# Kernel tuning notes

Measured on AMD Instinct MI355X. Metric: run time of the kernel, lower is better.

## Reference

```python
import jax, jax.numpy as jnp
import numpy as np

EPS = 1e-5

def layer_norm(x, g, b):
    mu = jnp.mean(x, axis=-1, keepdims=True)
    var = jnp.mean(jnp.square(x - mu), axis=-1, keepdims=True)
    return (x - mu) * jax.lax.rsqrt(var + EPS) * g + b

def setup_inputs() -> dict:
    key = jax.random.key(0)
    ks = jax.random.split(key, 10)
    B, V, S, D, H, FF = 4, 1024, 2048, 512, 8, 2048
    s = 0.02
    return {
        "tgt": jax.random.normal(ks[0], (B, V, D), jnp.float32),
        "memory": jax.random.normal(ks[1], (B, S, D), jnp.float32),
        "memory_key_padding_mask": jax.random.bernoulli(ks[2], 0.3, (B, S)),  # True = padding
        "Wq": jax.random.normal(ks[3], (D, D), jnp.float32) * s,
        "Wkv": jax.random.normal(ks[4], (2 * D, D), jnp.float32) * s,
        "Wo": jax.random.normal(ks[5], (D, D), jnp.float32) * s,
        "W1": jax.random.normal(ks[6], (FF, D), jnp.float32) * s,
        "b1": jnp.zeros((FF,), jnp.float32),
        "W2": jax.random.normal(ks[7], (D, FF), jnp.float32) * s,
        "b2": jnp.zeros((D,), jnp.float32),
        "g1": jnp.ones((D,), jnp.float32),
        "be1": jnp.zeros((D,), jnp.float32),
        "g2": jnp.ones((D,), jnp.float32),
        "be2": jnp.zeros((D,), jnp.float32),
    }

def reference(tgt, memory, memory_key_padding_mask, Wq, Wkv, Wo, W1, b1, W2, b2, g1, be1, g2, be2):
    B, V, D = tgt.shape
    S = memory.shape[1]
    H = 8
    hd = D // H
    # projections (no bias on q/kv/out per bias=False)
    q = (tgt @ Wq.T).reshape(B, V, H, hd)
    kv = (memory @ Wkv.T).reshape(B, S, 2, H, hd)
    k, v = kv[:, :, 0], kv[:, :, 1]
    # cross attention over valid (non-padded) context tokens only.
    # Equivalent math to flash-attn-varlen packing: padded keys get zero weight.
    scores = jnp.einsum("bqhd,bkhd->bhqk", q, k) / jnp.sqrt(jnp.asarray(hd, q.dtype))
    neg = jnp.finfo(scores.dtype).min
    scores = jnp.where(memory_key_padding_mask[:, None, None, :], neg, scores)
    attn = jax.nn.softmax(scores, axis=-1)
    attn_out = jnp.einsum("bhqk,bkhd->bqhd", attn, v).reshape(B, V, D)
    attn_out = attn_out @ Wo.T
    # post-norm scheme, dropout=0
    x = layer_norm(tgt + attn_out, g1, be1)
    ff = jax.nn.relu(x @ W1.T + b1) @ W2.T + b2
    return layer_norm(x + ff, g2, be2)
```

## Files before the change

### kernel.cpp

```cpp
#include <hip/hip_runtime.h>
#include <hip/hip_bf16.h>

typedef unsigned short u16;
typedef __attribute__((ext_vector_type(8))) short short8;
typedef __attribute__((ext_vector_type(4))) float floatx4;

#define AS1 __attribute__((address_space(1)))
#define AS3 __attribute__((address_space(3)))

__device__ __forceinline__ u16 f2bf(float f) {
  unsigned u = __float_as_uint(f);
  u = u + 0x7FFFu + ((u >> 16) & 1u);
  return (u16)(u >> 16);
}
__device__ __forceinline__ unsigned pack_bf2(float a, float b) {
  return (unsigned)f2bf(a) | ((unsigned)f2bf(b) << 16);
}

__global__ __launch_bounds__(256) void cast_bf16_kernel(const float* __restrict__ in,
                                                        u16* __restrict__ out, int n4) {
  int i = blockIdx.x * 256 + threadIdx.x;
  int stride = gridDim.x * 256;
  for (; i < n4; i += stride) {
    float4 v = reinterpret_cast<const float4*>(in)[i];
    ushort4 o;
    o.x = f2bf(v.x); o.y = f2bf(v.y); o.z = f2bf(v.z); o.w = f2bf(v.w);
    reinterpret_cast<ushort4*>(out)[i] = o;
  }
}

__global__ __launch_bounds__(256) void mask_bits_kernel(const void* __restrict__ mraw,
                                                        unsigned* __restrict__ mout, int n) {
  __shared__ int mode;
  const int t = threadIdx.x;
  const int* mi = (const int*)mraw;
  if (t == 0) mode = 0;
  __syncthreads();
  int local = 0;
  for (int i = t; i < 2048; i += 256) {
    unsigned v = (unsigned)mi[i];
    if (v == 0x3F800000u) { local = 2; break; }
    if (v > 1u) local = 1;
  }
  atomicMax(&mode, local);
  __syncthreads();
  const int m = mode;
  const unsigned char* mb = (const unsigned char*)mraw;
  const float* mf = (const float*)mraw;
  for (int wk = t; wk < n / 32; wk += 256) {
    unsigned bits = 0;
    for (int i = 0; i < 32; ++i) {
      int s = wk * 32 + i;
      int v;
      if (m == 1)      v = (int)mb[s];
      else if (m == 2) v = (mf[s] != 0.0f) ? 1 : 0;
      else             v = mi[s];
      bits |= (v ? 1u : 0u) << i;
    }
    mout[wk] = bits;
  }
}

template<int EPI>
__global__ __launch_bounds__(256) void gemm_bt(
    const u16* __restrict__ A, const u16* __restrict__ B, void* __restrict__ Cv,
    const float* __restrict__ bias,
    int M, int N, int K, int lda, int ldb, int ldc,
    long aBatch, long bBatch, long cBatch)
{
  __shared__ u16 As[2][128 * 32];
  __shared__ u16 Bs[2][128 * 32];
  const int t = threadIdx.x;
  const int l = t & 63;
  const int w = t >> 6;
  const int wr = w >> 1, wc = w & 1;
  const int m0 = blockIdx.y * 128, n0 = blockIdx.x * 128;
  const long z = blockIdx.z;
  const u16* Ab = A + z * aBatch;
  const u16* Bb = B + z * bBatch;

  floatx4 acc[4][4];
#pragma unroll
  for (int m = 0; m < 4; ++m)
#pragma unroll
    for (int n = 0; n < 4; ++n)
      acc[m][n] = (floatx4){0.f, 0.f, 0.f, 0.f};

  const int row_st = t >> 2;
  const int kcol = (t & 3) * 8;

  auto stage = [&](int buf, int kt) {
#pragma unroll
    for (int c = 0; c < 2; ++c) {
      int rA = m0 + c * 64 + row_st; if (rA >= M) rA = M - 1;
      int rB = n0 + c * 64 + row_st; if (rB >= N) rB = N - 1;
      int li = (c * 256 + t) * 8;
      __builtin_amdgcn_global_load_lds(
          (const AS1 void*)(Ab + (long)rA * lda + kt + kcol),
          (AS3 void*)(As[buf] + li), 16, 0, 0);
      __builtin_amdgcn_global_load_lds(
          (const AS1 void*)(Bb + (long)rB * ldb + kt + kcol),
          (AS3 void*)(Bs[buf] + li), 16, 0, 0);
    }
  };

  stage(0, 0);
  __syncthreads();
  int cur = 0;
  for (int kt = 0; kt < K; kt += 32) {
    if (kt + 32 < K) stage(cur ^ 1, kt + 32);

    short8 af[4], bf[4];
#pragma unroll
    for (int m = 0; m < 4; ++m)
      af[m] = *reinterpret_cast<const short8*>(&As[cur][(wr * 64 + m * 16 + (l & 15)) * 32 + (l >> 4) * 8]);
#pragma unroll
    for (int n = 0; n < 4; ++n)
      bf[n] = *reinterpret_cast<const short8*>(&Bs[cur][(wc * 64 + n * 16 + (l & 15)) * 32 + (l >> 4) * 8]);

    __builtin_amdgcn_s_setprio(1);
#pragma unroll
    for (int m = 0; m < 4; ++m)
#pragma unroll
      for (int n = 0; n < 4; ++n)
        acc[m][n] = __builtin_amdgcn_mfma_f32_16x16x32_bf16(af[m], bf[n], acc[m][n], 0, 0, 0);
    __builtin_amdgcn_s_setprio(0);

    __syncthreads();
    cur ^= 1;
  }

  const int cr = (l >> 4) * 4;
  const int cc = l & 15;
#pragma unroll
  for (int m = 0; m < 4; ++m) {
#pragma unroll
    for (int j = 0; j < 4; ++j) {
      int row = m0 + wr * 64 + m * 16 + cr + j;
      if (row < M) {
#pragma unroll
        for (int n = 0; n < 4; ++n) {
          int col = n0 + wc * 64 + n * 16 + cc;
          if (col < N) {
            float v = acc[m][n][j];
            long idx = z * cBatch + (long)row * ldc + col;
            if constexpr (EPI == 0) {
              ((u16*)Cv)[idx] = f2bf(v);
            } else if constexpr (EPI == 1) {
              ((float*)Cv)[idx] = v;
            } else if constexpr (EPI == 2) {
              v += bias[col]; v = fmaxf(v, 0.f);
              ((u16*)Cv)[idx] = f2bf(v);
            } else {
              v += bias[col];
              ((float*)Cv)[idx] = v;
            }
          }
        }
      }
    }
  }
}

__global__ __launch_bounds__(512, 4) void flash_attn_kernel(
    const u16* __restrict__ Qg, const u16* __restrict__ KVg,
    const u16* __restrict__ Vtg, const unsigned* __restrict__ mbits,
    u16* __restrict__ Og)
{
  __shared__ __align__(16) u16 KVbuf[2][2][64 * 64];
  __shared__ __align__(16) u16 Ps[8][32 * 32];
  __shared__ float mlred[2][2][128];
  __shared__ unsigned mw[64];

  const int t = threadIdx.x;
  const int l = t & 63;
  const int w = t >> 6;
  const int wr = w >> 1;
  const int wc = w & 1;
  const int lo = l & 15, hi = l >> 4;

  const int id = blockIdx.y * 8 + blockIdx.x;
  const int vid = (id & 7) * 32 + (id >> 3);
  const int qt = vid & 7, bh = vid >> 3;
  const int b = bh >> 3, h = bh & 7;

  const long qbase = ((long)b * 1024 + qt * 128) * 512 + h * 64;
  const long kbase = ((long)b * 2048) * 1024 + h * 64;
  const long vbase = ((long)bh * 64) * 2048;

  if (t < 64) mw[t] = mbits[b * 64 + t];

  auto stage_kv = [&](int buf, int soff) {
    const int s = t >> 3, c = t & 7;
    __builtin_amdgcn_global_load_lds(
        (const AS1 void*)(KVg + kbase + (long)(soff + s) * 1024 + ((c ^ (s & 7)) * 8)),
        (AS3 void*)(&KVbuf[buf][0][t * 8]), 16, 0, 0);
    __builtin_amdgcn_global_load_lds(
        (const AS1 void*)(Vtg + vbase + (long)s * 2048 + soff + ((c ^ (s & 7)) * 8)),
        (AS3 void*)(&KVbuf[buf][1][t * 8]), 16, 0, 0);
  };

  stage_kv(0, 0);

  short8 af[2][2];
#pragma unroll
  for (int qm = 0; qm < 2; ++qm)
#pragma unroll
    for (int ks = 0; ks < 2; ++ks)
      af[qm][ks] = *reinterpret_cast<const short8*>(
          Qg + qbase + (long)(wr * 32 + qm * 16 + lo) * 512 + ks * 32 + hi * 8);

  __syncthreads();

  floatx4 accO[4][2];
#pragma unroll
  for (int dn = 0; dn < 4; ++dn)
#pragma unroll
    for (int qm = 0; qm < 2; ++qm)
      accO[dn][qm] = (floatx4){0.f, 0.f, 0.f, 0.f};
  float m_run[2] = {-1.0e30f, -1.0e30f};
  float l_run[2] = {0.f, 0.f};

  int cur = 0;
  for (int it = 0; it < 32; ++it) {
    const int s0 = it * 64;
    if (it + 1 < 32) stage_kv(cur ^ 1, s0 + 64);

    short8 bfr[2][2];
#pragma unroll
    for (int sn = 0; sn < 2; ++sn)
#pragma unroll
      for (int ks = 0; ks < 2; ++ks) {
        const int srow = wc * 32 + sn * 16 + lo;
        bfr[sn][ks] = *reinterpret_cast<const short8*>(
            &KVbuf[cur][0][srow * 64 + (((ks * 4 + hi) ^ (lo & 7)) * 8)]);
      }
    floatx4 sacc[2][2];
#pragma unroll
    for (int sn = 0; sn < 2; ++sn)
#pragma unroll
      for (int qm = 0; qm < 2; ++qm)
        sacc[sn][qm] = (floatx4){0.f, 0.f, 0.f, 0.f};
    __builtin_amdgcn_s_setprio(1);
#pragma unroll
    for (int sn = 0; sn < 2; ++sn)
#pragma unroll
      for (int qm = 0; qm < 2; ++qm)
#pragma unroll
        for (int ks = 0; ks < 2; ++ks)
          sacc[sn][qm] = __builtin_amdgcn_mfma_f32_16x16x32_bf16(bfr[sn][ks], af[qm][ks], sacc[sn][qm], 0, 0, 0);
    __builtin_amdgcn_s_setprio(0);

    const unsigned mword = mw[it * 2 + wc];
#pragma unroll
    for (int sn = 0; sn < 2; ++sn) {
      const unsigned nib = (mword >> (sn * 16)) >> (hi * 4);
#pragma unroll
      for (int j = 0; j < 4; ++j) {
        const bool mk = (nib >> j) & 1u;
#pragma unroll
        for (int qm = 0; qm < 2; ++qm)
          sacc[sn][qm][j] = mk ? -3.0e38f : sacc[sn][qm][j] * 0.125f;
      }
    }

    float al[2];
#pragma unroll
    for (int qm = 0; qm < 2; ++qm) {
      float mx = fmaxf(fmaxf(fmaxf(sacc[0][qm][0], sacc[0][qm][1]), fmaxf(sacc[0][qm][2], sacc[0][qm][3])),
                       fmaxf(fmaxf(sacc[1][qm][0], sacc[1][qm][1]), fmaxf(sacc[1][qm][2], sacc[1][qm][3])));
      mx = fmaxf(mx, __shfl_xor(mx, 16));
      mx = fmaxf(mx, __shfl_xor(mx, 32));
      const float mn = fmaxf(m_run[qm], mx);
      al[qm] = __expf(m_run[qm] - mn);
      m_run[qm] = mn;
      l_run[qm] *= al[qm];
    }
#pragma unroll
    for (int dn = 0; dn < 4; ++dn)
#pragma unroll
      for (int qm = 0; qm < 2; ++qm)
#pragma unroll
        for (int j = 0; j < 4; ++j)
          accO[dn][qm][j] *= al[qm];

#pragma unroll
    for (int qm = 0; qm < 2; ++qm) {
      float s = 0.f;
      unsigned pw[2][2];
#pragma unroll
      for (int sn = 0; sn < 2; ++sn) {
        const float e0 = __expf(sacc[sn][qm][0] - m_run[qm]);
        const float e1 = __expf(sacc[sn][qm][1] - m_run[qm]);
        const float e2 = __expf(sacc[sn][qm][2] - m_run[qm]);
        const float e3 = __expf(sacc[sn][qm][3] - m_run[qm]);
        s += (e0 + e1) + (e2 + e3);
        pw[sn][0] = pack_bf2(e0, e1);
        pw[sn][1] = pack_bf2(e2, e3);
      }
      s += __shfl_xor(s, 16);
      s += __shfl_xor(s, 32);
      l_run[qm] += s;
      const int ql = qm * 16 + lo;
#pragma unroll
      for (int sn = 0; sn < 2; ++sn) {
        uint2 wv; wv.x = pw[sn][0]; wv.y = pw[sn][1];
        *reinterpret_cast<uint2*>(&Ps[w][ql * 32 + (((sn * 4 + hi) ^ (lo & 7)) * 4)]) = wv;
      }
    }

    short8 va[4];
#pragma unroll
    for (int dn = 0; dn < 4; ++dn) {
      const int d = dn * 16 + lo;
      va[dn] = *reinterpret_cast<const short8*>(
          &KVbuf[cur][1][d * 64 + (((wc * 4 + hi) ^ (d & 7)) * 8)]);
    }
    short8 pb[2];
#pragma unroll
    for (int qm = 0; qm < 2; ++qm) {
      const int ql = qm * 16 + lo;
      uint2 a = *reinterpret_cast<const uint2*>(&Ps[w][ql * 32 + (((2 * hi) ^ (lo & 7)) * 4)]);
      uint2 bq = *reinterpret_cast<const uint2*>(&Ps[w][ql * 32 + (((2 * hi + 1) ^ (lo & 7)) * 4)]);
      uint4 comb; comb.x = a.x; comb.y = a.y; comb.z = bq.x; comb.w = bq.y;
      __builtin_memcpy(&pb[qm], &comb, 16);
    }
    __builtin_amdgcn_s_setprio(1);
#pragma unroll
    for (int dn = 0; dn < 4; ++dn)
#pragma unroll
      for (int qm = 0; qm < 2; ++qm)
        accO[dn][qm] = __builtin_amdgcn_mfma_f32_16x16x32_bf16(va[dn], pb[qm], accO[dn][qm], 0, 0, 0);
    __builtin_amdgcn_s_setprio(0);

    __syncthreads();
    cur ^= 1;
  }

  if (hi == 0) {
#pragma unroll
    for (int qm = 0; qm < 2; ++qm) {
      const int q = wr * 32 + qm * 16 + lo;
      mlred[wc][0][q] = m_run[qm];
      mlred[wc][1][q] = l_run[qm];
    }
  }
  __syncthreads();
  float scal[2];
#pragma unroll
  for (int qm = 0; qm < 2; ++qm) {
    const int q = wr * 32 + qm * 16 + lo;
    const float ms = fmaxf(mlred[0][0][q], mlred[1][0][q]);
    scal[qm] = __expf(m_run[qm] - ms);
  }
  float* Of = (float*)KVbuf;
  if (wc == 0) {
#pragma unroll
    for (int dn = 0; dn < 4; ++dn)
#pragma unroll
      for (int qm = 0; qm < 2; ++qm) {
        const int q = wr * 32 + qm * 16 + lo;
        float4 v;
        v.x = accO[dn][qm][0] * scal[qm]; v.y = accO[dn][qm][1] * scal[qm];
        v.z = accO[dn][qm][2] * scal[qm]; v.w = accO[dn][qm][3] * scal[qm];
        *reinterpret_cast<float4*>(&Of[q * 64 + (((dn * 4 + hi) ^ (q & 15)) * 4)]) = v;
      }
  }
  __syncthreads();
  if (wc == 1) {
#pragma unroll
    for (int dn = 0; dn < 4; ++dn)
#pragma unroll
      for (int qm = 0; qm < 2; ++qm) {
        const int q = wr * 32 + qm * 16 + lo;
        float4* pp = reinterpret_cast<float4*>(&Of[q * 64 + (((dn * 4 + hi) ^ (q & 15)) * 4)]);
        float4 v = *pp;
        v.x += accO[dn][qm][0] * scal[qm]; v.y += accO[dn][qm][1] * scal[qm];
        v.z += accO[dn][qm][2] * scal[qm]; v.w += accO[dn][qm][3] * scal[qm];
        *pp = v;
      }
  }
  __syncthreads();
  {
    const int q = t >> 2;
    const float m0 = mlred[0][0][q], m1 = mlred[1][0][q];
    const float ms = fmaxf(m0, m1);
    const float ls = mlred[0][1][q] * __expf(m0 - ms) + mlred[1][1][q] * __expf(m1 - ms);
    const float inv = 1.0f / ls;
    u16 ov[16];
#pragma unroll
    for (int c4 = 0; c4 < 4; ++c4) {
      const int c = (t & 3) * 4 + c4;
      float4 v = *reinterpret_cast<const float4*>(&Of[q * 64 + ((c ^ (q & 15)) * 4)]);
      ov[c4 * 4 + 0] = f2bf(v.x * inv); ov[c4 * 4 + 1] = f2bf(v.y * inv);
      ov[c4 * 4 + 2] = f2bf(v.z * inv); ov[c4 * 4 + 3] = f2bf(v.w * inv);
    }
    u16* dst = Og + qbase + (long)q * 512 + (t & 3) * 16;
    uint4 w0, w1;
    __builtin_memcpy(&w0, &ov[0], 16);
    __builtin_memcpy(&w1, &ov[8], 16);
    *reinterpret_cast<uint4*>(dst) = w0;
    *reinterpret_cast<uint4*>(dst + 8) = w1;
  }
}

template<int P, bool WRITE_BF>
__global__ __launch_bounds__(64) void lnp_kernel(const float* __restrict__ r1,
    const float* __restrict__ parts, long pstride,
    const float* __restrict__ bias,
    const float* __restrict__ g, const float* __restrict__ be,
    float* __restrict__ xf, u16* __restrict__ xb) {
  const long base = (long)blockIdx.x * 512;
  const int t = threadIdx.x;
  float v[8]; float s = 0.f;
#pragma unroll
  for (int j = 0; j < 8; ++j) {
    int i = t + j * 64;
    float acc = r1[base + i] + (bias ? bias[i] : 0.f);
#pragma unroll
    for (int q = 0; q < P; ++q) acc += parts[q * pstride + base + i];
    v[j] = acc; s += acc;
  }
#pragma unroll
  for (int o = 32; o; o >>= 1) s += __shfl_xor(s, o);
  const float mu = s * (1.0f / 512.0f);
  float q2 = 0.f;
#pragma unroll
  for (int j = 0; j < 8; ++j) { float d = v[j] - mu; q2 += d * d; }
#pragma unroll
  for (int o = 32; o; o >>= 1) q2 += __shfl_xor(q2, o);
  const float rs = rsqrtf(q2 * (1.0f / 512.0f) + 1e-5f);
#pragma unroll
  for (int j = 0; j < 8; ++j) {
    int i = t + j * 64;
    float o = (v[j] - mu) * rs * g[i] + be[i];
    xf[base + i] = o;
    if (WRITE_BF) xb[base + i] = f2bf(o);
  }
}

__global__ __launch_bounds__(256) void transpose_v_kernel(const u16* __restrict__ KV,
                                                          u16* __restrict__ Vt) {
  __shared__ u16 tile[128 * 65];
  const int z = blockIdx.y;
  const int b = z >> 3, h = z & 7;
  const int s0 = blockIdx.x * 128;
  const int t = threadIdx.x;
#pragma unroll
  for (int k = 0; k < 32; ++k) {
    int i = k * 256 + t;
    int s = i >> 6, d = i & 63;
    tile[s * 65 + d] = KV[(long)(b * 2048 + s0 + s) * 1024 + 512 + h * 64 + d];
  }
  __syncthreads();
#pragma unroll
  for (int k = 0; k < 32; ++k) {
    int i = k * 256 + t;
    int d = i >> 7, sl = i & 127;
    Vt[((long)z * 64 + d) * 2048 + s0 + sl] = tile[sl * 65 + d];
  }
}

extern "C" void kernel_launch(void* const* d_in, const int* in_sizes, int n_in,
                              void* d_out, int out_size, void* d_ws, size_t ws_size,
                              hipStream_t stream) {
  const float* tgt    = (const float*)d_in[0];
  const float* memory = (const float*)d_in[1];
  const void*  maskraw= (const void*)d_in[2];
  const float* Wq  = (const float*)d_in[3];
  const float* Wkv = (const float*)d_in[4];
  const float* Wo  = (const float*)d_in[5];
  const float* W1  = (const float*)d_in[6];
  const float* b1  = (const float*)d_in[7];
  const float* W2  = (const float*)d_in[8];
  const float* b2  = (const float*)d_in[9];
  const float* g1  = (const float*)d_in[10];
  const float* be1 = (const float*)d_in[11];
  const float* g2  = (const float*)d_in[12];
  const float* be2 = (const float*)d_in[13];

  constexpr int B = 4, V = 1024, S = 2048, D = 512, H = 8, FF = 2048, hd = 64;
  const long BVD = (long)B * V * D;

  char* p = (char*)d_ws;
  auto alloc = [&](size_t bytes) -> void* {
    void* r = (void*)p; p += (bytes + 255) & ~(size_t)255; return r;
  };
  u16*  tgt_b = (u16*)alloc((size_t)B * V * D * 2);
  u16*  mem_b = (u16*)alloc((size_t)B * S * D * 2);
  u16*  wq_b  = (u16*)alloc((size_t)D * D * 2);
  u16*  wkv_b = (u16*)alloc((size_t)2 * D * D * 2);
  u16*  wo_b  = (u16*)alloc((size_t)D * D * 2);
  u16*  w1_b  = (u16*)alloc((size_t)FF * D * 2);
  u16*  w2_b  = (u16*)alloc((size_t)D * FF * 2);
  u16*  Qb    = (u16*)alloc((size_t)B * V * D * 2);
  u16*  KVb   = (u16*)alloc((size_t)B * S * 2 * D * 2);
  u16*  Vt    = (u16*)alloc((size_t)B * H * hd * S * 2);
  u16*  attn_b= (u16*)alloc((size_t)B * V * D * 2);
  float* projP = (float*)alloc((size_t)4 * BVD * 4);
  float* xf   = (float*)alloc((size_t)BVD * 4);
  u16*  xb    = (u16*)alloc((size_t)BVD * 2);
  u16*  hb    = (u16*)alloc((size_t)B * V * FF * 2);
  float* ffbP = (float*)alloc((size_t)4 * BVD * 4);
  unsigned* mbitsW = (unsigned*)alloc((size_t)(B * S / 32) * 4);

  auto cast = [&](const float* src, u16* dst, long n) {
    int n4 = (int)(n / 4);
    int grid = (n4 + 255) / 256; if (grid > 2048) grid = 2048; if (grid < 1) grid = 1;
    cast_bf16_kernel<<<dim3(grid), dim3(256), 0, stream>>>(src, dst, n4);
  };
  cast(tgt, tgt_b, (long)B * V * D);
  cast(memory, mem_b, (long)B * S * D);
  cast(Wq, wq_b, (long)D * D);
  cast(Wkv, wkv_b, (long)2 * D * D);
  cast(Wo, wo_b, (long)D * D);
  cast(W1, w1_b, (long)FF * D);
  cast(W2, w2_b, (long)D * FF);

  mask_bits_kernel<<<dim3(1), 256, 0, stream>>>(maskraw, mbitsW, B * S);

  gemm_bt<0><<<dim3(D / 128, (B * V) / 128, 1), 256, 0, stream>>>(
      tgt_b, wq_b, Qb, nullptr, B * V, D, D, D, D, D, 0, 0, 0);
  gemm_bt<0><<<dim3((2 * D) / 128, (B * S) / 128, 1), 256, 0, stream>>>(
      mem_b, wkv_b, KVb, nullptr, B * S, 2 * D, D, D, D, 2 * D, 0, 0, 0);
  transpose_v_kernel<<<dim3(S / 128, B * H), 256, 0, stream>>>(KVb, Vt);

  flash_attn_kernel<<<dim3(8, B * H), 512, 0, stream>>>(
      Qb, KVb, Vt, mbitsW, attn_b);

  gemm_bt<1><<<dim3(D / 128, (B * V) / 128, 4), 256, 0, stream>>>(
      attn_b, wo_b, projP, nullptr, B * V, D, D / 4, D, D, D,
      (long)(D / 4), (long)(D / 4), BVD);
  lnp_kernel<4, true><<<dim3(B * V), 64, 0, stream>>>(
      tgt, projP, BVD, nullptr, g1, be1, xf, xb);
  gemm_bt<2><<<dim3(FF / 128, (B * V) / 128, 1), 256, 0, stream>>>(
      xb, w1_b, hb, b1, B * V, FF, D, D, D, FF, 0, 0, 0);
  gemm_bt<1><<<dim3(D / 128, (B * V) / 128, 4), 256, 0, stream>>>(
      hb, w2_b, ffbP, nullptr, B * V, D, FF / 4, FF, FF, D,
      (long)(FF / 4), (long)(FF / 4), BVD);
  lnp_kernel<4, false><<<dim3(B * V), 64, 0, stream>>>(
      xf, ffbP, BVD, b2, g2, be2, (float*)d_out, nullptr);
}
```

Before: 302.8 us.

## Halve attention query tile, fold softmax scale into Q GEMM, merge cast launches

```diff
diff --git a/kernel.cpp b/kernel.cpp
--- a/kernel.cpp
+++ b/kernel.cpp
@@ -1,5 +1,4 @@
 #include <hip/hip_runtime.h>
-#include <hip/hip_bf16.h>
 
 typedef unsigned short u16;
 typedef __attribute__((ext_vector_type(8))) short short8;
@@ -17,15 +16,31 @@
   return (unsigned)f2bf(a) | ((unsigned)f2bf(b) << 16);
 }
 
-__global__ __launch_bounds__(256) void cast_bf16_kernel(const float* __restrict__ in,
-                                                        u16* __restrict__ out, int n4) {
+__global__ __launch_bounds__(256) void cast_all_kernel(
+    const float* __restrict__ s0, u16* __restrict__ d0,
+    const float* __restrict__ s1, u16* __restrict__ d1,
+    const float* __restrict__ s2, u16* __restrict__ d2,
+    const float* __restrict__ s3, u16* __restrict__ d3,
+    const float* __restrict__ s4, u16* __restrict__ d4,
+    const float* __restrict__ s5, u16* __restrict__ d5,
+    const float* __restrict__ s6, u16* __restrict__ d6)
+{
+  const int total = 2359296;
   int i = blockIdx.x * 256 + threadIdx.x;
-  int stride = gridDim.x * 256;
-  for (; i < n4; i += stride) {
-    float4 v = reinterpret_cast<const float4*>(in)[i];
+  const int stride = gridDim.x * 256;
+  for (; i < total; i += stride) {
+    const float* s; u16* d; int loc;
+    if (i < 524288)        { s = s0; d = d0; loc = i; }
+    else if (i < 1572864)  { s = s1; d = d1; loc = i - 524288; }
+    else if (i < 1638400)  { s = s2; d = d2; loc = i - 1572864; }
+    else if (i < 1769472)  { s = s3; d = d3; loc = i - 1638400; }
+    else if (i < 1835008)  { s = s4; d = d4; loc = i - 1769472; }
+    else if (i < 2097152)  { s = s5; d = d5; loc = i - 1835008; }
+    else                   { s = s6; d = d6; loc = i - 2097152; }
+    float4 v = reinterpret_cast<const float4*>(s)[loc];
     ushort4 o;
     o.x = f2bf(v.x); o.y = f2bf(v.y); o.z = f2bf(v.z); o.w = f2bf(v.w);
-    reinterpret_cast<ushort4*>(out)[i] = o;
+    reinterpret_cast<ushort4*>(d)[loc] = o;
   }
 }
 
@@ -45,17 +60,28 @@
   atomicMax(&mode, local);
   __syncthreads();
   const int m = mode;
-  const unsigned char* mb = (const unsigned char*)mraw;
-  const float* mf = (const float*)mraw;
-  for (int wk = t; wk < n / 32; wk += 256) {
+  const uint4* m4 = (const uint4*)mraw;
+  const int nw = n / 32;
+  for (int wk = t; wk < nw; wk += 256) {
     unsigned bits = 0;
-    for (int i = 0; i < 32; ++i) {
-      int s = wk * 32 + i;
-      int v;
-      if (m == 1)      v = (int)mb[s];
-      else if (m == 2) v = (mf[s] != 0.0f) ? 1 : 0;
-      else             v = mi[s];
-      bits |= (v ? 1u : 0u) << i;
+    if (m == 1) {
+      uint4 a = m4[wk * 2], b = m4[wk * 2 + 1];
+      unsigned ww[8] = {a.x, a.y, a.z, a.w, b.x, b.y, b.z, b.w};
+#pragma unroll
+      for (int k = 0; k < 8; ++k)
+#pragma unroll
+        for (int j = 0; j < 4; ++j)
+          bits |= (((ww[k] >> (j * 8)) & 0xFFu) ? 1u : 0u) << (k * 4 + j);
+    } else {
+#pragma unroll
+      for (int k = 0; k < 8; ++k) {
+        uint4 a = m4[wk * 8 + k];
+        unsigned t0 = (m == 2) ? ((a.x << 1) ? 1u : 0u) : (a.x ? 1u : 0u);
+        unsigned t1 = (m == 2) ? ((a.y << 1) ? 1u : 0u) : (a.y ? 1u : 0u);
+        unsigned t2 = (m == 2) ? ((a.z << 1) ? 1u : 0u) : (a.z ? 1u : 0u);
+        unsigned t3 = (m == 2) ? ((a.w << 1) ? 1u : 0u) : (a.w ? 1u : 0u);
+        bits |= (t0 | (t1 << 1) | (t2 << 2) | (t3 << 3)) << (k * 4);
+      }
     }
     mout[wk] = bits;
   }
@@ -92,9 +118,9 @@
   auto stage = [&](int buf, int kt) {
 #pragma unroll
     for (int c = 0; c < 2; ++c) {
-      int rA = m0 + c * 64 + row_st; if (rA >= M) rA = M - 1;
-      int rB = n0 + c * 64 + row_st; if (rB >= N) rB = N - 1;
-      int li = (c * 256 + t) * 8;
+      const int rA = m0 + c * 64 + row_st;
+      const int rB = n0 + c * 64 + row_st;
+      const int li = (c * 256 + t) * 8;
       __builtin_amdgcn_global_load_lds(
           (const AS1 void*)(Ab + (long)rA * lda + kt + kcol),
           (AS3 void*)(As[buf] + li), 16, 0, 0);
@@ -136,26 +162,24 @@
   for (int m = 0; m < 4; ++m) {
 #pragma unroll
     for (int j = 0; j < 4; ++j) {
-      int row = m0 + wr * 64 + m * 16 + cr + j;
-      if (row < M) {
-#pragma unroll
-        for (int n = 0; n < 4; ++n) {
-          int col = n0 + wc * 64 + n * 16 + cc;
-          if (col < N) {
-            float v = acc[m][n][j];
-            long idx = z * cBatch + (long)row * ldc + col;
-            if constexpr (EPI == 0) {
-              ((u16*)Cv)[idx] = f2bf(v);
-            } else if constexpr (EPI == 1) {
-              ((float*)Cv)[idx] = v;
-            } else if constexpr (EPI == 2) {
-              v += bias[col]; v = fmaxf(v, 0.f);
-              ((u16*)Cv)[idx] = f2bf(v);
-            } else {
-              v += bias[col];
-              ((float*)Cv)[idx] = v;
-            }
-          }
+      const int row = m0 + wr * 64 + m * 16 + cr + j;
+#pragma unroll
+      for (int n = 0; n < 4; ++n) {
+        const int col = n0 + wc * 64 + n * 16 + cc;
+        float v = acc[m][n][j];
+        long idx = z * cBatch + (long)row * ldc + col;
+        if constexpr (EPI == 0) {
+          ((u16*)Cv)[idx] = f2bf(v);
+        } else if constexpr (EPI == 1) {
+          ((float*)Cv)[idx] = v;
+        } else if constexpr (EPI == 2) {
+          v += bias[col]; v = fmaxf(v, 0.f);
+          ((u16*)Cv)[idx] = f2bf(v);
+        } else if constexpr (EPI == 3) {
+          v += bias[col];
+          ((float*)Cv)[idx] = v;
+        } else {
+          ((u16*)Cv)[idx] = f2bf(v * 0.125f);
         }
       }
     }
@@ -168,8 +192,8 @@
     u16* __restrict__ Og)
 {
   __shared__ __align__(16) u16 KVbuf[2][2][64 * 64];
-  __shared__ __align__(16) u16 Ps[8][32 * 32];
-  __shared__ float mlred[2][2][128];
+  __shared__ __align__(16) u16 Ps[8][16 * 32];
+  __shared__ float mlred[2][2][64];
   __shared__ unsigned mw[64];
 
   const int t = threadIdx.x;
@@ -179,12 +203,12 @@
   const int wc = w & 1;
   const int lo = l & 15, hi = l >> 4;
 
-  const int id = blockIdx.y * 8 + blockIdx.x;
-  const int vid = (id & 7) * 32 + (id >> 3);
-  const int qt = vid & 7, bh = vid >> 3;
+  const int id = blockIdx.y * 16 + blockIdx.x;
+  const int vid = (id & 7) * 64 + (id >> 3);
+  const int qt = vid & 15, bh = vid >> 4;
   const int b = bh >> 3, h = bh & 7;
 
-  const long qbase = ((long)b * 1024 + qt * 128) * 512 + h * 64;
+  const long qbase = ((long)b * 1024 + qt * 64) * 512 + h * 64;
   const long kbase = ((long)b * 2048) * 1024 + h * 64;
   const long vbase = ((long)bh * 64) * 2048;
 
@@ -202,24 +226,19 @@
 
   stage_kv(0, 0);
 
-  short8 af[2][2];
-#pragma unroll
-  for (int qm = 0; qm < 2; ++qm)
-#pragma unroll
-    for (int ks = 0; ks < 2; ++ks)
-      af[qm][ks] = *reinterpret_cast<const short8*>(
-          Qg + qbase + (long)(wr * 32 + qm * 16 + lo) * 512 + ks * 32 + hi * 8);
-
-  __syncthreads();
-
-  floatx4 accO[4][2];
+  short8 af[2];
+#pragma unroll
+  for (int ks = 0; ks < 2; ++ks)
+    af[ks] = *reinterpret_cast<const short8*>(
+        Qg + qbase + (long)(wr * 16 + lo) * 512 + ks * 32 + hi * 8);
+
+  __syncthreads();
+
+  floatx4 accO[4];
 #pragma unroll
   for (int dn = 0; dn < 4; ++dn)
-#pragma unroll
-    for (int qm = 0; qm < 2; ++qm)
-      accO[dn][qm] = (floatx4){0.f, 0.f, 0.f, 0.f};
-  float m_run[2] = {-1.0e30f, -1.0e30f};
-  float l_run[2] = {0.f, 0.f};
+    accO[dn] = (floatx4){0.f, 0.f, 0.f, 0.f};
+  float m_run = -1.0e30f, l_run = 0.f;
 
   int cur = 0;
   for (int it = 0; it < 32; ++it) {
@@ -235,20 +254,16 @@
         bfr[sn][ks] = *reinterpret_cast<const short8*>(
             &KVbuf[cur][0][srow * 64 + (((ks * 4 + hi) ^ (lo & 7)) * 8)]);
       }
-    floatx4 sacc[2][2];
+    floatx4 sacc[2];
 #pragma unroll
     for (int sn = 0; sn < 2; ++sn)
-#pragma unroll
-      for (int qm = 0; qm < 2; ++qm)
-        sacc[sn][qm] = (floatx4){0.f, 0.f, 0.f, 0.f};
+      sacc[sn] = (floatx4){0.f, 0.f, 0.f, 0.f};
     __builtin_amdgcn_s_setprio(1);
 #pragma unroll
     for (int sn = 0; sn < 2; ++sn)
 #pragma unroll
-      for (int qm = 0; qm < 2; ++qm)
-#pragma unroll
-        for (int ks = 0; ks < 2; ++ks)
-          sacc[sn][qm] = __builtin_amdgcn_mfma_f32_16x16x32_bf16(bfr[sn][ks], af[qm][ks], sacc[sn][qm], 0, 0, 0);
+      for (int ks = 0; ks < 2; ++ks)
+        sacc[sn] = __builtin_amdgcn_mfma_f32_16x16x32_bf16(bfr[sn][ks], af[ks], sacc[sn], 0, 0, 0);
     __builtin_amdgcn_s_setprio(0);
 
     const unsigned mword = mw[it * 2 + wc];
@@ -256,56 +271,44 @@
     for (int sn = 0; sn < 2; ++sn) {
       const unsigned nib = (mword >> (sn * 16)) >> (hi * 4);
 #pragma unroll
-      for (int j = 0; j < 4; ++j) {
-        const bool mk = (nib >> j) & 1u;
-#pragma unroll
-        for (int qm = 0; qm < 2; ++qm)
-          sacc[sn][qm][j] = mk ? -3.0e38f : sacc[sn][qm][j] * 0.125f;
-      }
-    }
-
-    float al[2];
-#pragma unroll
-    for (int qm = 0; qm < 2; ++qm) {
-      float mx = fmaxf(fmaxf(fmaxf(sacc[0][qm][0], sacc[0][qm][1]), fmaxf(sacc[0][qm][2], sacc[0][qm][3])),
-                       fmaxf(fmaxf(sacc[1][qm][0], sacc[1][qm][1]), fmaxf(sacc[1][qm][2], sacc[1][qm][3])));
-      mx = fmaxf(mx, __shfl_xor(mx, 16));
-      mx = fmaxf(mx, __shfl_xor(mx, 32));
-      const float mn = fmaxf(m_run[qm], mx);
-      al[qm] = __expf(m_run[qm] - mn);
-      m_run[qm] = mn;
-      l_run[qm] *= al[qm];
-    }
+      for (int j = 0; j < 4; ++j)
+        if ((nib >> j) & 1u) sacc[sn][j] = -3.0e38f;
+    }
+
+    float mx = fmaxf(fmaxf(fmaxf(sacc[0][0], sacc[0][1]), fmaxf(sacc[0][2], sacc[0][3])),
+                     fmaxf(fmaxf(sacc[1][0], sacc[1][1]), fmaxf(sacc[1][2], sacc[1][3])));
+    mx = fmaxf(mx, __shfl_xor(mx, 16));
+    mx = fmaxf(mx, __shfl_xor(mx, 32));
+    const float mn = fmaxf(m_run, mx);
+    const float al = __expf(m_run - mn);
+    m_run = mn;
+    l_run *= al;
 #pragma unroll
     for (int dn = 0; dn < 4; ++dn)
 #pragma unroll
-      for (int qm = 0; qm < 2; ++qm)
-#pragma unroll
-        for (int j = 0; j < 4; ++j)
-          accO[dn][qm][j] *= al[qm];
-
-#pragma unroll
-    for (int qm = 0; qm < 2; ++qm) {
+      for (int j = 0; j < 4; ++j)
+        accO[dn][j] *= al;
+
+    {
       float s = 0.f;
       unsigned pw[2][2];
 #pragma unroll
       for (int sn = 0; sn < 2; ++sn) {
-        const float e0 = __expf(sacc[sn][qm][0] - m_run[qm]);
-        const float e1 = __expf(sacc[sn][qm][1] - m_run[qm]);
-        const float e2 = __expf(sacc[sn][qm][2] - m_run[qm]);
-        const float e3 = __expf(sacc[sn][qm][3] - m_run[qm]);
+        const float e0 = __expf(sacc[sn][0] - m_run);
+        const float e1 = __expf(sacc[sn][1] - m_run);
+        const float e2 = __expf(sacc[sn][2] - m_run);
+        const float e3 = __expf(sacc[sn][3] - m_run);
         s += (e0 + e1) + (e2 + e3);
         pw[sn][0] = pack_bf2(e0, e1);
         pw[sn][1] = pack_bf2(e2, e3);
       }
       s += __shfl_xor(s, 16);
       s += __shfl_xor(s, 32);
-      l_run[qm] += s;
-      const int ql = qm * 16 + lo;
+      l_run += s;
 #pragma unroll
       for (int sn = 0; sn < 2; ++sn) {
         uint2 wv; wv.x = pw[sn][0]; wv.y = pw[sn][1];
-        *reinterpret_cast<uint2*>(&Ps[w][ql * 32 + (((sn * 4 + hi) ^ (lo & 7)) * 4)]) = wv;
+        *reinterpret_cast<uint2*>(&Ps[w][lo * 32 + (((sn * 4 + hi) ^ (lo & 7)) * 4)]) = wv;
       }
     }
 
@@ -316,21 +319,17 @@
       va[dn] = *reinterpret_cast<const short8*>(
           &KVbuf[cur][1][d * 64 + (((wc * 4 + hi) ^ (d & 7)) * 8)]);
     }
-    short8 pb[2];
-#pragma unroll
-    for (int qm = 0; qm < 2; ++qm) {
-      const int ql = qm * 16 + lo;
-      uint2 a = *reinterpret_cast<const uint2*>(&Ps[w][ql * 32 + (((2 * hi) ^ (lo & 7)) * 4)]);
-      uint2 bq = *reinterpret_cast<const uint2*>(&Ps[w][ql * 32 + (((2 * hi + 1) ^ (lo & 7)) * 4)]);
+    short8 pb;
+    {
+      uint2 a = *reinterpret_cast<const uint2*>(&Ps[w][lo * 32 + (((2 * hi) ^ (lo & 7)) * 4)]);
+      uint2 bq = *reinterpret_cast<const uint2*>(&Ps[w][lo * 32 + (((2 * hi + 1) ^ (lo & 7)) * 4)]);
       uint4 comb; comb.x = a.x; comb.y = a.y; comb.z = bq.x; comb.w = bq.y;
-      __builtin_memcpy(&pb[qm], &comb, 16);
+      __builtin_memcpy(&pb, &comb, 16);
     }
     __builtin_amdgcn_s_setprio(1);
 #pragma unroll
     for (int dn = 0; dn < 4; ++dn)
-#pragma unroll
-      for (int qm = 0; qm < 2; ++qm)
-        accO[dn][qm] = __builtin_amdgcn_mfma_f32_16x16x32_bf16(va[dn], pb[qm], accO[dn][qm], 0, 0, 0);
+      accO[dn] = __builtin_amdgcn_mfma_f32_16x16x32_bf16(va[dn], pb, accO[dn], 0, 0, 0);
     __builtin_amdgcn_s_setprio(0);
 
     __syncthreads();
@@ -338,69 +337,58 @@
   }
 
   if (hi == 0) {
-#pragma unroll
-    for (int qm = 0; qm < 2; ++qm) {
-      const int q = wr * 32 + qm * 16 + lo;
-      mlred[wc][0][q] = m_run[qm];
-      mlred[wc][1][q] = l_run[qm];
-    }
-  }
-  __syncthreads();
-  float scal[2];
-#pragma unroll
-  for (int qm = 0; qm < 2; ++qm) {
-    const int q = wr * 32 + qm * 16 + lo;
+    const int q = wr * 16 + lo;
+    mlred[wc][0][q] = m_run;
+    mlred[wc][1][q] = l_run;
+  }
+  __syncthreads();
+  float scal;
+  {
+    const int q = wr * 16 + lo;
     const float ms = fmaxf(mlred[0][0][q], mlred[1][0][q]);
-    scal[qm] = __expf(m_run[qm] - ms);
+    scal = __expf(m_run - ms);
   }
   float* Of = (float*)KVbuf;
   if (wc == 0) {
 #pragma unroll
-    for (int dn = 0; dn < 4; ++dn)
-#pragma unroll
-      for (int qm = 0; qm < 2; ++qm) {
-        const int q = wr * 32 + qm * 16 + lo;
-        float4 v;
-        v.x = accO[dn][qm][0] * scal[qm]; v.y = accO[dn][qm][1] * scal[qm];
-        v.z = accO[dn][qm][2] * scal[qm]; v.w = accO[dn][qm][3] * scal[qm];
-        *reinterpret_cast<float4*>(&Of[q * 64 + (((dn * 4 + hi) ^ (q & 15)) * 4)]) = v;
-      }
+    for (int dn = 0; dn < 4; ++dn) {
+      const int q = wr * 16 + lo;
+      float4 v;
+      v.x = accO[dn][0] * scal; v.y = accO[dn][1] * scal;
+      v.z = accO[dn][2] * scal; v.w = accO[dn][3] * scal;
+      *reinterpret_cast<float4*>(&Of[q * 64 + (((dn * 4 + hi) ^ (q & 15)) * 4)]) = v;
+    }
   }
   __syncthreads();
   if (wc == 1) {
 #pragma unroll
-    for (int dn = 0; dn < 4; ++dn)
-#pragma unroll
-      for (int qm = 0; qm < 2; ++qm) {
-        const int q = wr * 32 + qm * 16 + lo;
-        float4* pp = reinterpret_cast<float4*>(&Of[q * 64 + (((dn * 4 + hi) ^ (q & 15)) * 4)]);
-        float4 v = *pp;
-        v.x += accO[dn][qm][0] * scal[qm]; v.y += accO[dn][qm][1] * scal[qm];
-        v.z += accO[dn][qm][2] * scal[qm]; v.w += accO[dn][qm][3] * scal[qm];
-        *pp = v;
-      }
+    for (int dn = 0; dn < 4; ++dn) {
+      const int q = wr * 16 + lo;
+      float4* pp = reinterpret_cast<float4*>(&Of[q * 64 + (((dn * 4 + hi) ^ (q & 15)) * 4)]);
+      float4 v = *pp;
+      v.x += accO[dn][0] * scal; v.y += accO[dn][1] * scal;
+      v.z += accO[dn][2] * scal; v.w += accO[dn][3] * scal;
+      *pp = v;
+    }
   }
   __syncthreads();
   {
-    const int q = t >> 2;
+    const int q = t >> 3;
+    const int dc = t & 7;
     const float m0 = mlred[0][0][q], m1 = mlred[1][0][q];
     const float ms = fmaxf(m0, m1);
     const float ls = mlred[0][1][q] * __expf(m0 - ms) + mlred[1][1][q] * __expf(m1 - ms);
     const float inv = 1.0f / ls;
-    u16 ov[16];
-#pragma unroll
-    for (int c4 = 0; c4 < 4; ++c4) {
-      const int c = (t & 3) * 4 + c4;
-      float4 v = *reinterpret_cast<const float4*>(&Of[q * 64 + ((c ^ (q & 15)) * 4)]);
-      ov[c4 * 4 + 0] = f2bf(v.x * inv); ov[c4 * 4 + 1] = f2bf(v.y * inv);
-      ov[c4 * 4 + 2] = f2bf(v.z * inv); ov[c4 * 4 + 3] = f2bf(v.w * inv);
-    }
-    u16* dst = Og + qbase + (long)q * 512 + (t & 3) * 16;
-    uint4 w0, w1;
-    __builtin_memcpy(&w0, &ov[0], 16);
-    __builtin_memcpy(&w1, &ov[8], 16);
-    *reinterpret_cast<uint4*>(dst) = w0;
-    *reinterpret_cast<uint4*>(dst + 8) = w1;
+    float4 v0 = *reinterpret_cast<const float4*>(&Of[q * 64 + (((dc * 2) ^ (q & 15)) * 4)]);
+    float4 v1 = *reinterpret_cast<const float4*>(&Of[q * 64 + (((dc * 2 + 1) ^ (q & 15)) * 4)]);
+    u16 ov[8];
+    ov[0] = f2bf(v0.x * inv); ov[1] = f2bf(v0.y * inv);
+    ov[2] = f2bf(v0.z * inv); ov[3] = f2bf(v0.w * inv);
+    ov[4] = f2bf(v1.x * inv); ov[5] = f2bf(v1.y * inv);
+    ov[6] = f2bf(v1.z * inv); ov[7] = f2bf(v1.w * inv);
+    uint4 wv;
+    __builtin_memcpy(&wv, ov, 16);
+    *reinterpret_cast<uint4*>(Og + qbase + (long)q * 512 + dc * 8) = wv;
   }
 }
 
@@ -504,28 +492,18 @@
   float* ffbP = (float*)alloc((size_t)4 * BVD * 4);
   unsigned* mbitsW = (unsigned*)alloc((size_t)(B * S / 32) * 4);
 
-  auto cast = [&](const float* src, u16* dst, long n) {
-    int n4 = (int)(n / 4);
-    int grid = (n4 + 255) / 256; if (grid > 2048) grid = 2048; if (grid < 1) grid = 1;
-    cast_bf16_kernel<<<dim3(grid), dim3(256), 0, stream>>>(src, dst, n4);
-  };
-  cast(tgt, tgt_b, (long)B * V * D);
-  cast(memory, mem_b, (long)B * S * D);
-  cast(Wq, wq_b, (long)D * D);
-  cast(Wkv, wkv_b, (long)2 * D * D);
-  cast(Wo, wo_b, (long)D * D);
-  cast(W1, w1_b, (long)FF * D);
-  cast(W2, w2_b, (long)D * FF);
+  cast_all_kernel<<<dim3(2048), 256, 0, stream>>>(
+      tgt, tgt_b, memory, mem_b, Wq, wq_b, Wkv, wkv_b, Wo, wo_b, W1, w1_b, W2, w2_b);
 
   mask_bits_kernel<<<dim3(1), 256, 0, stream>>>(maskraw, mbitsW, B * S);
 
-  gemm_bt<0><<<dim3(D / 128, (B * V) / 128, 1), 256, 0, stream>>>(
+  gemm_bt<4><<<dim3(D / 128, (B * V) / 128, 1), 256, 0, stream>>>(
       tgt_b, wq_b, Qb, nullptr, B * V, D, D, D, D, D, 0, 0, 0);
   gemm_bt<0><<<dim3((2 * D) / 128, (B * S) / 128, 1), 256, 0, stream>>>(
       mem_b, wkv_b, KVb, nullptr, B * S, 2 * D, D, D, D, 2 * D, 0, 0, 0);
   transpose_v_kernel<<<dim3(S / 128, B * H), 256, 0, stream>>>(KVb, Vt);
 
-  flash_attn_kernel<<<dim3(8, B * H), 512, 0, stream>>>(
+  flash_attn_kernel<<<dim3(16, B * H), 512, 0, stream>>>(
       Qb, KVb, Vt, mbitsW, attn_b);
 
   gemm_bt<1><<<dim3(D / 128, (B * V) / 128, 4), 256, 0, stream>>>(
```

After: 268.5 us. 11.4% less time.
